# Optimization experiments

Measured on AMD Instinct MI355X. Metric: run time of the kernel, lower is better.

The kernel has to match this reference:

```python
import jax, jax.numpy as jnp
import numpy as np

N_NODES = 100000
N_EDGES = 1600000
F_IN = 128
F_HID = 128
N_CLASSES = 40
PERIODS = 1


def gcn_conv(x, edge_index, edge_weight, W, b):
    """PyG GCNConv: add self-loops (weight 1), symmetric normalization, scatter-add aggregation."""
    N = x.shape[0]
    row, col = edge_index[0], edge_index[1]
    loop = jnp.arange(N)
    row_f = jnp.concatenate([row, loop])
    col_f = jnp.concatenate([col, loop])
    w_f = jnp.concatenate([edge_weight, jnp.ones((N,), dtype=x.dtype)])
    deg = jax.ops.segment_sum(w_f, col_f, num_segments=N)
    dinv = jnp.where(deg > 0, jax.lax.rsqrt(deg), jnp.zeros_like(deg))
    norm = dinv[row_f] * w_f * dinv[col_f]            # [E+N]
    xw = x @ W                                        # [N, F_out]
    msg = norm[:, None] * xw[row_f]                   # [E+N, F_out] gather
    out = jax.ops.segment_sum(msg, col_f, num_segments=N)  # scatter-add
    return out + b


def setup_inputs() -> dict:
    key = jax.random.key(0)
    ks = jax.random.split(key, 8)
    x = jax.random.normal(ks[0], (N_NODES, F_IN), dtype=jnp.float32)
    edge_index = jax.random.randint(ks[1], (2, N_EDGES), 0, N_NODES, dtype=jnp.int64)
    edge_weight = jax.random.uniform(ks[2], (N_EDGES,), dtype=jnp.float32)
    attention = jax.random.uniform(ks[3], (PERIODS,), dtype=jnp.float32)
    W1 = jax.random.normal(ks[4], (F_IN, F_HID), dtype=jnp.float32) * (1.0 / np.sqrt(F_IN))
    b1 = jnp.zeros((F_HID,), dtype=jnp.float32)
    W2 = jax.random.normal(ks[5], (F_HID, N_CLASSES), dtype=jnp.float32) * (1.0 / np.sqrt(F_HID))
    b2 = jnp.zeros((N_CLASSES,), dtype=jnp.float32)
    return {"x": x, "edge_index": edge_index, "edge_weight": edge_weight,
            "attention": attention, "W1": W1, "b1": b1, "W2": W2, "b2": b2}


def reference(x, edge_index, edge_weight, attention, W1, b1, W2, b2):
    periods = attention.shape[0]
    h0 = x.reshape(x.shape[0], x.shape[1], 1)          # matches x.view(N, F, 1)
    probs = jax.nn.softmax(attention, axis=0)
    H_accum = 0.0
    for period in range(periods):                      # periods == 1 structurally
        H_accum = H_accum + probs[period] * gcn_conv(h0[:, :, period], edge_index, edge_weight, W1, b1)
    h = jax.nn.relu(H_accum)
    h = gcn_conv(h, edge_index, edge_weight, W2, b2)
    return jax.nn.softmax(h, axis=1)
```

## Files before the change

### kernel.cpp

```cpp
#include <hip/hip_runtime.h>
#include <hip/hip_bf16.h>
#include <hip/hip_fp16.h>

#define N_NODES 100000
#define N_EDGES 1600000
#define G1_BLOCKS 782


__global__ void init_kernel(unsigned long long* packed) {
    int i = blockIdx.x * 256 + threadIdx.x;
    if (i < N_NODES) packed[i] = 0ULL;
}


__global__ __launch_bounds__(256) void k1_kernel(const float* __restrict__ X,
                                                 const float* __restrict__ W,
                                                 __half* __restrict__ XW,
                                                 const int* __restrict__ ei,
                                                 const float* __restrict__ ew,
                                                 unsigned long long* packed,
                                                 int* __restrict__ seq) {
    __shared__ float sA[32][132];
    __shared__ float sB[32][132];
    int t = threadIdx.x;
    if (blockIdx.x >= G1_BLOCKS) {
        int e = (blockIdx.x - G1_BLOCKS) * 256 + t;
        if (e < N_EDGES) {
            int c = ei[N_EDGES + e];
            unsigned int fw = (unsigned int)rintf(ew[e] * 1048576.0f);
            unsigned long long old = atomicAdd(&packed[c], (1ULL << 32) | (unsigned long long)fw);
            seq[e] = (int)(old >> 32);
        }
        return;
    }
    int row0 = blockIdx.x * 128;
    int tc = t & 15, tr = t >> 4;
    int m0 = tr * 8, n0 = tc * 8;
    float acc[8][8] = {};
    for (int kt = 0; kt < 128; kt += 32) {
        #pragma unroll
        for (int q = 0; q < 4; ++q) {
            int g = t + q * 256;
            int row = g >> 3;
            int c4 = g & 7;
            float4 v = make_float4(0.f, 0.f, 0.f, 0.f);
            int grow = row0 + row;
            if (grow < N_NODES) v = *(const float4*)(X + (size_t)grow * 128 + kt + c4 * 4);
            sA[c4 * 4 + 0][row] = v.x;
            sA[c4 * 4 + 1][row] = v.y;
            sA[c4 * 4 + 2][row] = v.z;
            sA[c4 * 4 + 3][row] = v.w;
        }
        #pragma unroll
        for (int q = 0; q < 4; ++q) {
            int g = t + q * 256;
            int k = g >> 5, n4 = g & 31;
            *(float4*)(&sB[k][n4 * 4]) = *(const float4*)(W + (kt + k) * 128 + n4 * 4);
        }
        __syncthreads();
        #pragma unroll
        for (int k = 0; k < 32; ++k) {
            float4 a0 = *(const float4*)(&sA[k][m0]);
            float4 a1 = *(const float4*)(&sA[k][m0 + 4]);
            float4 b0 = *(const float4*)(&sB[k][n0]);
            float4 b1v = *(const float4*)(&sB[k][n0 + 4]);
            float a[8] = {a0.x, a0.y, a0.z, a0.w, a1.x, a1.y, a1.z, a1.w};
            float b[8] = {b0.x, b0.y, b0.z, b0.w, b1v.x, b1v.y, b1v.z, b1v.w};
            #pragma unroll
            for (int j = 0; j < 8; ++j)
                #pragma unroll
                for (int i = 0; i < 8; ++i) acc[j][i] += a[j] * b[i];
        }
        __syncthreads();
    }
    #pragma unroll
    for (int j = 0; j < 8; ++j) {
        int grow = row0 + m0 + j;
        if (grow < N_NODES) {
            __align__(16) __half2 hp[4];
            hp[0] = __floats2half2_rn(acc[j][0], acc[j][1]);
            hp[1] = __floats2half2_rn(acc[j][2], acc[j][3]);
            hp[2] = __floats2half2_rn(acc[j][4], acc[j][5]);
            hp[3] = __floats2half2_rn(acc[j][6], acc[j][7]);
            *(float4*)(XW + (size_t)grow * 128 + n0) = *(const float4*)hp;
        }
    }
}

__global__ void scanA_kernel(const unsigned long long* __restrict__ packed,
                             int* __restrict__ off, int* __restrict__ bsum,
                             float* __restrict__ dinv) {
    __shared__ int s[1024];
    int t = threadIdx.x;
    int i = blockIdx.x * 1024 + t;
    unsigned long long pk = (i < N_NODES) ? packed[i] : 0ULL;
    int v = (int)(pk >> 32);
    if (i < N_NODES) {
        float deg = 1.0f + (float)(unsigned int)(pk & 0xffffffffULL) * (1.0f / 1048576.0f);
        dinv[i] = rsqrtf(deg);
    }
    s[t] = v; __syncthreads();
    #pragma unroll
    for (int d = 1; d < 1024; d <<= 1) {
        int x = (t >= d) ? s[t - d] : 0;
        __syncthreads();
        s[t] += x;
        __syncthreads();
    }
    if (i < N_NODES) off[i] = s[t] - v;
    if (t == 1023) bsum[blockIdx.x] = s[1023];
}

__global__ void scanB_kernel(int* bsum, int nb) {
    __shared__ int s[1024];
    int t = threadIdx.x;
    int v = (t < nb) ? bsum[t] : 0;
    s[t] = v; __syncthreads();
    #pragma unroll
    for (int d = 1; d < 1024; d <<= 1) {
        int x = (t >= d) ? s[t - d] : 0;
        __syncthreads();
        s[t] += x;
        __syncthreads();
    }
    if (t < nb) bsum[t] = s[t] - v;
}

__global__ void scanC_kernel(int* __restrict__ off, const int* __restrict__ bsum) {
    int i = blockIdx.x * 1024 + threadIdx.x;
    if (i < N_NODES) off[i] += bsum[blockIdx.x];
    if (i == 0) off[N_NODES] = N_EDGES;
}

__global__ void fill_kernel(const int* __restrict__ ei, const float* __restrict__ w,
                            const float* __restrict__ dinv, const int* __restrict__ off,
                            const int* __restrict__ seq, int2* __restrict__ epack) {
    int e = blockIdx.x * 256 + threadIdx.x;
    if (e < N_EDGES) {
        int r = ei[e];
        int c = ei[N_EDGES + e];
        int p = off[c] + seq[e];
        float nrm = dinv[r] * w[e] * dinv[c];
        epack[p] = make_int2(r, __float_as_int(nrm));
    }
}


__global__ __launch_bounds__(256) void agg1f_kernel(const __half* __restrict__ XW,
                                                    const int* __restrict__ off,
                                                    const int2* __restrict__ epack,
                                                    const float* __restrict__ dinv,
                                                    const float* __restrict__ b1,
                                                    const float* __restrict__ W2,
                                                    __half* __restrict__ HW) {
    __shared__ __align__(16) float sW2[5120];
    __shared__ __align__(16) float sH[4][128];
    int t = threadIdx.x;
    #pragma unroll
    for (int q = 0; q < 5; ++q) {
        int g = t + q * 256;
        ((float4*)sW2)[g] = ((const float4*)W2)[g];
    }

    int wv = __builtin_amdgcn_readfirstlane(t) >> 6;
    int n = blockIdx.x * 4 + wv;
    int l = t & 63;
    const __half2* XW2 = (const __half2*)XW;
    float di = dinv[n];
    float self = di * di;
    float2 v = __half22float2(XW2[(size_t)n * 64 + l]);
    float accx[8], accy[8];
    accx[0] = self * v.x; accy[0] = self * v.y;
    #pragma unroll
    for (int k = 1; k < 8; ++k) { accx[k] = 0.f; accy[k] = 0.f; }
    int e0 = off[n], e1 = off[n + 1];
    int base = e0;
    for (; base + 16 <= e1; base += 16) {
        int2 p[16];
        #pragma unroll
        for (int k = 0; k < 16; ++k) p[k] = epack[base + k];
        #pragma unroll
        for (int k = 0; k < 16; ++k) {
            float2 g = __half22float2(XW2[(size_t)p[k].x * 64 + l]);
            float w = __int_as_float(p[k].y);
            accx[k & 7] += w * g.x;
            accy[k & 7] += w * g.y;
        }
    }
    for (; base < e1; base += 8) {
        int last = e1 - 1;
        int2 p[8];
        float w[8];
        #pragma unroll
        for (int k = 0; k < 8; ++k) {
            int e = base + k;
            int idx = min(e, last);
            p[k] = epack[idx];
            w[k] = (e < e1) ? __int_as_float(p[k].y) : 0.f;
        }
        #pragma unroll
        for (int k = 0; k < 8; ++k) {
            float2 g = __half22float2(XW2[(size_t)p[k].x * 64 + l]);
            accx[k] += w[k] * g.x;
            accy[k] += w[k] * g.y;
        }
    }
    float ax = ((accx[0] + accx[1]) + (accx[2] + accx[3])) + ((accx[4] + accx[5]) + (accx[6] + accx[7]));
    float ay = ((accy[0] + accy[1]) + (accy[2] + accy[3])) + ((accy[4] + accy[5]) + (accy[6] + accy[7]));
    float2 bb = ((const float2*)b1)[l];
    float hx = fmaxf(ax + bb.x, 0.f);
    float hy = fmaxf(ay + bb.y, 0.f);
    ((float2*)sH[wv])[l] = make_float2(hx, hy);
    __syncthreads();

    if (l < 40) {
        const float* hrow = sH[wv];
        float dot = 0.f;
        #pragma unroll 4
        for (int k = 0; k < 128; k += 4) {
            float4 h4 = *(const float4*)(hrow + k);
            dot += h4.x * sW2[(k + 0) * 40 + l];
            dot += h4.y * sW2[(k + 1) * 40 + l];
            dot += h4.z * sW2[(k + 2) * 40 + l];
            dot += h4.w * sW2[(k + 3) * 40 + l];
        }
        HW[(size_t)n * 40 + l] = __float2half_rn(dot);
    }
}


__global__ __launch_bounds__(256) void agg2_kernel(const __half* __restrict__ HW,
                                                   const int* __restrict__ off,
                                                   const int2* __restrict__ epack,
                                                   const float* __restrict__ dinv,
                                                   const float* __restrict__ b2,
                                                   float* __restrict__ out) {
    int t = threadIdx.x;
    int wv = __builtin_amdgcn_readfirstlane(t) >> 6;
    int n = blockIdx.x * 4 + wv;
    int l = t & 63;
    if (n >= N_NODES) return;
    bool act = (l < 40);
    int ll = act ? l : l - 40;
    float di = dinv[n];
    float acc[8];
    acc[0] = di * di * __half2float(HW[(size_t)n * 40 + ll]);
    #pragma unroll
    for (int k = 1; k < 8; ++k) acc[k] = 0.f;
    int e0 = off[n], e1 = off[n + 1];
    int base = e0;
    for (; base + 16 <= e1; base += 16) {
        int2 p[16];
        #pragma unroll
        for (int k = 0; k < 16; ++k) p[k] = epack[base + k];
        #pragma unroll
        for (int k = 0; k < 16; ++k) {
            float g = __half2float(HW[(size_t)p[k].x * 40 + ll]);
            acc[k & 7] += __int_as_float(p[k].y) * g;
        }
    }
    for (; base < e1; base += 8) {
        int last = e1 - 1;
        int2 p[8];
        float w[8];
        #pragma unroll
        for (int k = 0; k < 8; ++k) {
            int e = base + k;
            int idx = min(e, last);
            p[k] = epack[idx];
            w[k] = (e < e1) ? __int_as_float(p[k].y) : 0.f;
        }
        #pragma unroll
        for (int k = 0; k < 8; ++k) {
            float g = __half2float(HW[(size_t)p[k].x * 40 + ll]);
            acc[k] += w[k] * g;
        }
    }
    float a = ((acc[0] + acc[1]) + (acc[2] + acc[3])) + ((acc[4] + acc[5]) + (acc[6] + acc[7]));
    a += b2[ll];
    float m = act ? a : -1e30f;
    #pragma unroll
    for (int d = 32; d; d >>= 1) m = fmaxf(m, __shfl_xor(m, d, 64));
    float pexp = act ? expf(a - m) : 0.f;
    float s = pexp;
    #pragma unroll
    for (int d = 32; d; d >>= 1) s += __shfl_xor(s, d, 64);
    if (act) out[(size_t)n * 40 + l] = pexp / s;
}


extern "C" void kernel_launch(void* const* d_in, const int* in_sizes, int n_in,
                              void* d_out, int out_size, void* d_ws, size_t ws_size,
                              hipStream_t stream) {
    const float* x  = (const float*)d_in[0];
    const int*   ei = (const int*)d_in[1];
    const float* ew = (const float*)d_in[2];
    const float* W1 = (const float*)d_in[4];
    const float* b1 = (const float*)d_in[5];
    const float* W2 = (const float*)d_in[6];
    const float* b2 = (const float*)d_in[7];
    float* out = (float*)d_out;

    char* p = (char*)d_ws;
    auto alloc = [&](size_t bytes) -> void* {
        void* r = (void*)p;
        p += (bytes + 511) & ~(size_t)511;
        return r;
    };
    unsigned long long* packed = (unsigned long long*)alloc((size_t)N_NODES * 8);
    float* dinv   = (float*)alloc((size_t)N_NODES * 4);
    int*   off    = (int*)alloc((size_t)(N_NODES + 1) * 4);
    int*   bsum   = (int*)alloc(1024 * 4);
    int*   seq    = (int*)alloc((size_t)N_EDGES * 4);
    int2*  epack  = (int2*)alloc((size_t)N_EDGES * 8);
    __half* XW    = (__half*)alloc((size_t)N_NODES * 128 * 2);
    __half* HW    = (__half*)alloc((size_t)N_NODES * 40 * 2);

    int nblk_n = (N_NODES + 255) / 256;
    int nblk_e = (N_EDGES + 255) / 256;
    int nblk_s = (N_NODES + 1023) / 1024;

    hipLaunchKernelGGL(init_kernel,  dim3(nblk_n), dim3(256), 0, stream, packed);
    hipLaunchKernelGGL(k1_kernel,    dim3(G1_BLOCKS + nblk_e), dim3(256), 0, stream,
                       x, W1, XW, ei, ew, packed, seq);
    hipLaunchKernelGGL(scanA_kernel, dim3(nblk_s), dim3(1024), 0, stream, packed, off, bsum, dinv);
    hipLaunchKernelGGL(scanB_kernel, dim3(1), dim3(1024), 0, stream, bsum, nblk_s);
    hipLaunchKernelGGL(scanC_kernel, dim3(nblk_s), dim3(1024), 0, stream, off, bsum);
    hipLaunchKernelGGL(fill_kernel,  dim3(nblk_e), dim3(256), 0, stream, ei, ew, dinv, off, seq, epack);

    hipLaunchKernelGGL(agg1f_kernel, dim3(N_NODES / 4), dim3(256), 0, stream,
                       XW, off, epack, dinv, b1, W2, HW);
    hipLaunchKernelGGL(agg2_kernel,  dim3((N_NODES + 3) / 4), dim3(256), 0, stream,
                       HW, off, epack, dinv, b2, out);
}
```

Before: 281.2 us.

## Vectorize edge counting and CSR fill, process two nodes per wave in agg1

The edge-counting branch of k1 now handles 8 edges per thread with int4/float4 loads and vectorized seq stores. The CSR fill kernel handles 4 edges per thread with vector loads and batched gathers. agg1f now has each wave aggregate two consecutive nodes interleaved, which gives more independent gathers in flight and halves the block count, amortizing the per-block W2 shared-memory load. The cost is higher register pressure and padded iterations when the two nodes' degrees differ.

```diff
diff --git a/kernel.cpp b/kernel.cpp
--- a/kernel.cpp
+++ b/kernel.cpp
@@ -5,6 +5,7 @@
 #define N_NODES 100000
 #define N_EDGES 1600000
 #define G1_BLOCKS 782
+#define CNT_BLOCKS 782
 
 
 __global__ void init_kernel(unsigned long long* packed) {
@@ -24,12 +25,24 @@
     __shared__ float sB[32][132];
     int t = threadIdx.x;
     if (blockIdx.x >= G1_BLOCKS) {
-        int e = (blockIdx.x - G1_BLOCKS) * 256 + t;
-        if (e < N_EDGES) {
-            int c = ei[N_EDGES + e];
-            unsigned int fw = (unsigned int)rintf(ew[e] * 1048576.0f);
-            unsigned long long old = atomicAdd(&packed[c], (1ULL << 32) | (unsigned long long)fw);
-            seq[e] = (int)(old >> 32);
+        int base = ((blockIdx.x - G1_BLOCKS) * 256 + t) * 8;
+        if (base < N_EDGES) {
+            int4 c0 = *(const int4*)(ei + N_EDGES + base);
+            int4 c1 = *(const int4*)(ei + N_EDGES + base + 4);
+            float4 w0 = *(const float4*)(ew + base);
+            float4 w1 = *(const float4*)(ew + base + 4);
+            int c[8] = {c0.x, c0.y, c0.z, c0.w, c1.x, c1.y, c1.z, c1.w};
+            float wv[8] = {w0.x, w0.y, w0.z, w0.w, w1.x, w1.y, w1.z, w1.w};
+            int s[8];
+            #pragma unroll
+            for (int k = 0; k < 8; ++k) {
+                unsigned int fw = (unsigned int)rintf(wv[k] * 1048576.0f);
+                unsigned long long old =
+                    atomicAdd(&packed[c[k]], (1ULL << 32) | (unsigned long long)fw);
+                s[k] = (int)(old >> 32);
+            }
+            *(int4*)(seq + base)     = make_int4(s[0], s[1], s[2], s[3]);
+            *(int4*)(seq + base + 4) = make_int4(s[4], s[5], s[6], s[7]);
         }
         return;
     }
@@ -135,13 +148,24 @@
 __global__ void fill_kernel(const int* __restrict__ ei, const float* __restrict__ w,
                             const float* __restrict__ dinv, const int* __restrict__ off,
                             const int* __restrict__ seq, int2* __restrict__ epack) {
-    int e = blockIdx.x * 256 + threadIdx.x;
-    if (e < N_EDGES) {
-        int r = ei[e];
-        int c = ei[N_EDGES + e];
-        int p = off[c] + seq[e];
-        float nrm = dinv[r] * w[e] * dinv[c];
-        epack[p] = make_int2(r, __float_as_int(nrm));
+    int base = (blockIdx.x * 256 + threadIdx.x) * 4;
+    if (base >= N_EDGES) return;
+    int4 r4 = *(const int4*)(ei + base);
+    int4 c4 = *(const int4*)(ei + N_EDGES + base);
+    float4 w4 = *(const float4*)(w + base);
+    int4 s4 = *(const int4*)(seq + base);
+    int r[4] = {r4.x, r4.y, r4.z, r4.w};
+    int c[4] = {c4.x, c4.y, c4.z, c4.w};
+    float ww[4] = {w4.x, w4.y, w4.z, w4.w};
+    int s[4] = {s4.x, s4.y, s4.z, s4.w};
+    float dr[4], dc[4];
+    int ob[4];
+    #pragma unroll
+    for (int k = 0; k < 4; ++k) { dr[k] = dinv[r[k]]; dc[k] = dinv[c[k]]; ob[k] = off[c[k]]; }
+    #pragma unroll
+    for (int k = 0; k < 4; ++k) {
+        float nrm = dr[k] * ww[k] * dc[k];
+        epack[ob[k] + s[k]] = make_int2(r[k], __float_as_int(nrm));
     }
 }
 
@@ -154,7 +178,7 @@
                                                     const float* __restrict__ W2,
                                                     __half* __restrict__ HW) {
     __shared__ __align__(16) float sW2[5120];
-    __shared__ __align__(16) float sH[4][128];
+    __shared__ __align__(16) float sH[8][128];
     int t = threadIdx.x;
     #pragma unroll
     for (int q = 0; q < 5; ++q) {
@@ -163,68 +187,75 @@
     }
 
     int wv = __builtin_amdgcn_readfirstlane(t) >> 6;
-    int n = blockIdx.x * 4 + wv;
+    int nA = blockIdx.x * 8 + wv * 2;
+    int nB = nA + 1;
     int l = t & 63;
     const __half2* XW2 = (const __half2*)XW;
-    float di = dinv[n];
-    float self = di * di;
-    float2 v = __half22float2(XW2[(size_t)n * 64 + l]);
-    float accx[8], accy[8];
-    accx[0] = self * v.x; accy[0] = self * v.y;
-    #pragma unroll
-    for (int k = 1; k < 8; ++k) { accx[k] = 0.f; accy[k] = 0.f; }
-    int e0 = off[n], e1 = off[n + 1];
-    int base = e0;
-    for (; base + 16 <= e1; base += 16) {
-        int2 p[16];
-        #pragma unroll
-        for (int k = 0; k < 16; ++k) p[k] = epack[base + k];
+    float dA = dinv[nA], dB = dinv[nB];
+    float2 vA = __half22float2(XW2[(size_t)nA * 64 + l]);
+    float2 vB = __half22float2(XW2[(size_t)nB * 64 + l]);
+    float ax[8], ay[8], bx[8], by[8];
+    ax[0] = dA * dA * vA.x; ay[0] = dA * dA * vA.y;
+    bx[0] = dB * dB * vB.x; by[0] = dB * dB * vB.y;
+    #pragma unroll
+    for (int k = 1; k < 8; ++k) { ax[k] = 0.f; ay[k] = 0.f; bx[k] = 0.f; by[k] = 0.f; }
+    int e0A = off[nA], e1A = off[nA + 1], e1B = off[nB + 1];
+    int e0B = e1A;
+    int lenA = e1A - e0A, lenB = e1B - e0B;
+    int lastA = max(e1A - 1, 0);
+    int lastB = max(e1B - 1, 0);
+    int iters = (max(lenA, lenB) + 15) >> 4;
+    for (int it = 0; it < iters; ++it) {
+        int baseA = e0A + (it << 4);
+        int baseB = e0B + (it << 4);
+        int2 pA[16], pB[16];
+        float wA[16], wB[16];
         #pragma unroll
         for (int k = 0; k < 16; ++k) {
-            float2 g = __half22float2(XW2[(size_t)p[k].x * 64 + l]);
-            float w = __int_as_float(p[k].y);
-            accx[k & 7] += w * g.x;
-            accy[k & 7] += w * g.y;
-        }
-    }
-    for (; base < e1; base += 8) {
-        int last = e1 - 1;
-        int2 p[8];
-        float w[8];
-        #pragma unroll
-        for (int k = 0; k < 8; ++k) {
-            int e = base + k;
-            int idx = min(e, last);
-            p[k] = epack[idx];
-            w[k] = (e < e1) ? __int_as_float(p[k].y) : 0.f;
-        }
-        #pragma unroll
-        for (int k = 0; k < 8; ++k) {
-            float2 g = __half22float2(XW2[(size_t)p[k].x * 64 + l]);
-            accx[k] += w[k] * g.x;
-            accy[k] += w[k] * g.y;
-        }
-    }
-    float ax = ((accx[0] + accx[1]) + (accx[2] + accx[3])) + ((accx[4] + accx[5]) + (accx[6] + accx[7]));
-    float ay = ((accy[0] + accy[1]) + (accy[2] + accy[3])) + ((accy[4] + accy[5]) + (accy[6] + accy[7]));
+            int eA = baseA + k;
+            int iA = min(eA, lastA);
+            pA[k] = epack[iA];
+            wA[k] = (eA < e1A) ? __int_as_float(pA[k].y) : 0.f;
+        }
+        #pragma unroll
+        for (int k = 0; k < 16; ++k) {
+            int eB = baseB + k;
+            int iB = min(eB, lastB);
+            pB[k] = epack[iB];
+            wB[k] = (eB < e1B) ? __int_as_float(pB[k].y) : 0.f;
+        }
+        #pragma unroll
+        for (int k = 0; k < 16; ++k) {
+            float2 gA = __half22float2(XW2[(size_t)pA[k].x * 64 + l]);
+            float2 gB = __half22float2(XW2[(size_t)pB[k].x * 64 + l]);
+            ax[k & 7] += wA[k] * gA.x; ay[k & 7] += wA[k] * gA.y;
+            bx[k & 7] += wB[k] * gB.x; by[k & 7] += wB[k] * gB.y;
+        }
+    }
+    float axs = ((ax[0] + ax[1]) + (ax[2] + ax[3])) + ((ax[4] + ax[5]) + (ax[6] + ax[7]));
+    float ays = ((ay[0] + ay[1]) + (ay[2] + ay[3])) + ((ay[4] + ay[5]) + (ay[6] + ay[7]));
+    float bxs = ((bx[0] + bx[1]) + (bx[2] + bx[3])) + ((bx[4] + bx[5]) + (bx[6] + bx[7]));
+    float bys = ((by[0] + by[1]) + (by[2] + by[3])) + ((by[4] + by[5]) + (by[6] + by[7]));
     float2 bb = ((const float2*)b1)[l];
-    float hx = fmaxf(ax + bb.x, 0.f);
-    float hy = fmaxf(ay + bb.y, 0.f);
-    ((float2*)sH[wv])[l] = make_float2(hx, hy);
+    ((float2*)sH[wv * 2 + 0])[l] = make_float2(fmaxf(axs + bb.x, 0.f), fmaxf(ays + bb.y, 0.f));
+    ((float2*)sH[wv * 2 + 1])[l] = make_float2(fmaxf(bxs + bb.x, 0.f), fmaxf(bys + bb.y, 0.f));
     __syncthreads();
 
     if (l < 40) {
-        const float* hrow = sH[wv];
-        float dot = 0.f;
-        #pragma unroll 4
-        for (int k = 0; k < 128; k += 4) {
-            float4 h4 = *(const float4*)(hrow + k);
-            dot += h4.x * sW2[(k + 0) * 40 + l];
-            dot += h4.y * sW2[(k + 1) * 40 + l];
-            dot += h4.z * sW2[(k + 2) * 40 + l];
-            dot += h4.w * sW2[(k + 3) * 40 + l];
-        }
-        HW[(size_t)n * 40 + l] = __float2half_rn(dot);
+        #pragma unroll
+        for (int r = 0; r < 2; ++r) {
+            const float* hrow = sH[wv * 2 + r];
+            float dot = 0.f;
+            #pragma unroll 4
+            for (int k = 0; k < 128; k += 4) {
+                float4 h4 = *(const float4*)(hrow + k);
+                dot += h4.x * sW2[(k + 0) * 40 + l];
+                dot += h4.y * sW2[(k + 1) * 40 + l];
+                dot += h4.z * sW2[(k + 2) * 40 + l];
+                dot += h4.w * sW2[(k + 3) * 40 + l];
+            }
+            HW[(size_t)(nA + r) * 40 + l] = __float2half_rn(dot);
+        }
     }
 }
 
@@ -317,18 +348,18 @@
     __half* HW    = (__half*)alloc((size_t)N_NODES * 40 * 2);
 
     int nblk_n = (N_NODES + 255) / 256;
-    int nblk_e = (N_EDGES + 255) / 256;
+    int nblk_f = (N_EDGES / 4 + 255) / 256;
     int nblk_s = (N_NODES + 1023) / 1024;
 
     hipLaunchKernelGGL(init_kernel,  dim3(nblk_n), dim3(256), 0, stream, packed);
-    hipLaunchKernelGGL(k1_kernel,    dim3(G1_BLOCKS + nblk_e), dim3(256), 0, stream,
+    hipLaunchKernelGGL(k1_kernel,    dim3(G1_BLOCKS + CNT_BLOCKS), dim3(256), 0, stream,
                        x, W1, XW, ei, ew, packed, seq);
     hipLaunchKernelGGL(scanA_kernel, dim3(nblk_s), dim3(1024), 0, stream, packed, off, bsum, dinv);
     hipLaunchKernelGGL(scanB_kernel, dim3(1), dim3(1024), 0, stream, bsum, nblk_s);
     hipLaunchKernelGGL(scanC_kernel, dim3(nblk_s), dim3(1024), 0, stream, off, bsum);
-    hipLaunchKernelGGL(fill_kernel,  dim3(nblk_e), dim3(256), 0, stream, ei, ew, dinv, off, seq, epack);
-
-    hipLaunchKernelGGL(agg1f_kernel, dim3(N_NODES / 4), dim3(256), 0, stream,
+    hipLaunchKernelGGL(fill_kernel,  dim3(nblk_f), dim3(256), 0, stream, ei, ew, dinv, off, seq, epack);
+
+    hipLaunchKernelGGL(agg1f_kernel, dim3(N_NODES / 8), dim3(256), 0, stream,
                        XW, off, epack, dinv, b1, W2, HW);
     hipLaunchKernelGGL(agg2_kernel,  dim3((N_NODES + 3) / 4), dim3(256), 0, stream,
                        HW, off, epack, dinv, b2, out);
```

After: 293.1 us. 1.04x slower.
